# Kernel tuning notes

Hardware: AMD Instinct MI355X
Metric: run time of the kernel (lower is better)

## Reference

```python
import jax, jax.numpy as jnp
import numpy as np

L, B, F, D = 12, 2048, 6144, 768

def setup_inputs() -> dict:
    key = jax.random.key(0)
    k1, k2, k3 = jax.random.split(key, 3)
    acts = jax.random.normal(k1, (L, B, F), dtype=jnp.float32)
    # decoder weights for target layer: stacked per source layer, [L, F, D]
    W = jax.random.normal(k2, (L, F, D), dtype=jnp.float32) * 0.02
    bias = jax.random.normal(k3, (L, D), dtype=jnp.float32) * 0.01
    return {"acts": acts, "W": W, "bias": bias, "layer_idx": 11}

def reference(acts, W, bias, layer_idx):
    # decode(): sum over src_layer <= layer_idx of Linear(a[src], W[src->tgt], b[src->tgt])
    n = layer_idx + 1  # static Python int -> static slice
    a = acts[:n]       # [n, B, F]
    w = W[:n]          # [n, F, D]
    b = bias[:n]       # [n, D]
    # fused accumulation of all per-source-layer GEMMs
    recon = jnp.einsum('lbf,lfd->bd', a, w) + jnp.sum(b, axis=0)  # [B, D]
    return recon
```

## Files before the change

### kernel.cpp

```cpp
#include <hip/hip_runtime.h>
#include <hip/hip_bf16.h>

#define NB 2048
#define NF 6144
#define ND 768

typedef __attribute__((ext_vector_type(4))) __bf16 bf16x4;
typedef __attribute__((ext_vector_type(8))) __bf16 bf16x8;
typedef __attribute__((ext_vector_type(4))) float f32x4;

__global__ __launch_bounds__(256) void bias_init_kernel(
    const float* __restrict__ bias, const int* __restrict__ lidx,
    float* __restrict__ out) {
  int n = lidx[0] + 1;
  int i = blockIdx.x * 256 + threadIdx.x;
  if (i >= NB * ND) return;
  int d = i % ND;
  float s = 0.f;
  for (int l = 0; l < n; ++l) s += bias[l * ND + d];
  out[i] = s;
}

__global__ __launch_bounds__(256) void gemm_kernel(
    const float* __restrict__ acts, const float* __restrict__ W,
    const int* __restrict__ lidx, float* __restrict__ out) {
  const int l = blockIdx.z;
  if (l > lidx[0]) return;

  const int brow = blockIdx.x * 128;
  const int ncol = blockIdx.y * 128;

  __shared__ char cA[128 * 128];
  __shared__ char cB[128 * 128];

  const int tid = threadIdx.x;
  const int lane = tid & 63;
  const int wid = tid >> 6;
  const int wrow = (wid >> 1) * 64;
  const int wcol = (wid & 1) * 64;

  f32x4 acc[4][4];
#pragma unroll
  for (int i = 0; i < 4; ++i)
#pragma unroll
    for (int j = 0; j < 4; ++j) acc[i][j] = (f32x4){0.f, 0.f, 0.f, 0.f};

  const int arow = tid >> 4;
  const int ak = (tid & 15) * 4;
  const int bd = tid & 127;
  const int bkb0 = tid >> 7;

  const float* Aptr = acts + (size_t)l * NB * NF + (size_t)(brow + arow) * NF + ak;
  const float* Bptr = W + (size_t)l * NF * ND + (size_t)(bkb0 * 8) * ND + (ncol + bd);

  const int blkA = (ak >> 3) ^ (arow & 7);
  char* wA = cA + arow * 128 + (blkA << 4) + ((ak & 7) << 1);

  for (int kt = 0; kt < NF / 64; ++kt) {
    float4 av[8];
#pragma unroll
    for (int p = 0; p < 8; ++p)
      av[p] = *(const float4*)(Aptr + (size_t)p * (16 * NF));

    float bv[4][8];
#pragma unroll
    for (int p = 0; p < 4; ++p)
#pragma unroll
      for (int j = 0; j < 8; ++j)
        bv[p][j] = Bptr[(size_t)(p * 16 + j) * ND];

    __syncthreads();

#pragma unroll
    for (int p = 0; p < 8; ++p) {
      bf16x4 h;
      h[0] = (__bf16)av[p].x; h[1] = (__bf16)av[p].y;
      h[2] = (__bf16)av[p].z; h[3] = (__bf16)av[p].w;
      *(bf16x4*)(wA + p * 2048) = h;
    }
#pragma unroll
    for (int p = 0; p < 4; ++p) {
      const int kb8 = bkb0 + 2 * p;
      bf16x8 h;
#pragma unroll
      for (int j = 0; j < 8; ++j) h[j] = (__bf16)bv[p][j];
      *(bf16x8*)(cB + bd * 128 + ((kb8 ^ (bd & 7)) << 4)) = h;
    }

    __syncthreads();

#pragma unroll
    for (int s = 0; s < 2; ++s) {
      const int kb = s * 4 + (lane >> 4);
      bf16x8 aF[4], bF[4];
#pragma unroll
      for (int mi = 0; mi < 4; ++mi) {
        const int row = wrow + mi * 16 + (lane & 15);
        aF[mi] = *(const bf16x8*)(cA + row * 128 + ((kb ^ (row & 7)) << 4));
      }
#pragma unroll
      for (int ni = 0; ni < 4; ++ni) {
        const int row = wcol + ni * 16 + (lane & 15);
        bF[ni] = *(const bf16x8*)(cB + row * 128 + ((kb ^ (row & 7)) << 4));
      }
#pragma unroll
      for (int mi = 0; mi < 4; ++mi)
#pragma unroll
        for (int ni = 0; ni < 4; ++ni)
          acc[mi][ni] = __builtin_amdgcn_mfma_f32_16x16x32_bf16(
              aF[mi], bF[ni], acc[mi][ni], 0, 0, 0);
    }

    Aptr += 64;
    Bptr += (size_t)64 * ND;
  }

  const int orow = brow + wrow + ((lane >> 4) << 2);
  const int ocol = ncol + wcol + (lane & 15);
#pragma unroll
  for (int mi = 0; mi < 4; ++mi)
#pragma unroll
    for (int ni = 0; ni < 4; ++ni)
#pragma unroll
      for (int j = 0; j < 4; ++j)
        atomicAdd(out + (size_t)(orow + mi * 16 + j) * ND + (ocol + ni * 16),
                  acc[mi][ni][j]);
}

extern "C" void kernel_launch(void* const* d_in, const int* in_sizes, int n_in,
                              void* d_out, int out_size, void* d_ws, size_t ws_size,
                              hipStream_t stream) {
  const float* acts = (const float*)d_in[0];
  const float* W    = (const float*)d_in[1];
  const float* bias = (const float*)d_in[2];
  const int*   lidx = (const int*)d_in[3];
  float* out = (float*)d_out;

  const int L = in_sizes[0] / (NB * NF);

  bias_init_kernel<<<dim3((NB * ND + 255) / 256), 256, 0, stream>>>(bias, lidx, out);
  gemm_kernel<<<dim3(NB / 128, ND / 128, L), 256, 0, stream>>>(acts, W, lidx, out);
}
```

Measured before the change: 562.4 us.

## Software-pipeline global loads, vectorize W loads, and rework LDS swizzle

Global loads for the next K tile are issued right after the current tile is written to LDS, so they overlap with the MFMA compute instead of sitting in front of it. W is now read as float4 along the D dimension and transposed in registers, replacing scalar strided loads. A-tile stores widen to bf16x8. The LDS swizzle gains an extra XOR term, and launch bounds request two blocks per SIMD. The cost is that prefetch registers stay live across the compute loop, which adds register pressure.

Result: no change. 562.4 us (+0.0%).

```diff
diff --git a/kernel.cpp b/kernel.cpp
--- a/kernel.cpp
+++ b/kernel.cpp
@@ -4,10 +4,15 @@
 #define NB 2048
 #define NF 6144
 #define ND 768
+#define NT (NF / 64)
 
-typedef __attribute__((ext_vector_type(4))) __bf16 bf16x4;
 typedef __attribute__((ext_vector_type(8))) __bf16 bf16x8;
 typedef __attribute__((ext_vector_type(4))) float f32x4;
+
+__device__ __forceinline__ char* lds_addr(char* base, int row, int k) {
+  const int blk = ((k >> 3) ^ (row & 7) ^ ((row >> 2) & 7)) & 7;
+  return base + row * 128 + (blk << 4) + ((k & 7) << 1);
+}
 
 __global__ __launch_bounds__(256) void bias_init_kernel(
     const float* __restrict__ bias, const int* __restrict__ lidx,
@@ -21,7 +26,7 @@
   out[i] = s;
 }
 
-__global__ __launch_bounds__(256) void gemm_kernel(
+__global__ __launch_bounds__(256, 2) void gemm_kernel(
     const float* __restrict__ acts, const float* __restrict__ W,
     const int* __restrict__ lidx, float* __restrict__ out) {
   const int l = blockIdx.z;
@@ -45,64 +50,67 @@
 #pragma unroll
     for (int j = 0; j < 4; ++j) acc[i][j] = (f32x4){0.f, 0.f, 0.f, 0.f};
 
-  const int arow = tid >> 4;
-  const int ak = (tid & 15) * 4;
-  const int bd = tid & 127;
-  const int bkb0 = tid >> 7;
+  const int s_arow = tid >> 3;
+  const int s_ak = (tid & 7) * 8;
+  const int s_bd = (tid & 31) * 4;
+  const int s_bk = (tid >> 5) * 8;
 
-  const float* Aptr = acts + (size_t)l * NB * NF + (size_t)(brow + arow) * NF + ak;
-  const float* Bptr = W + (size_t)l * NF * ND + (size_t)(bkb0 * 8) * ND + (ncol + bd);
+  const float* Aptr =
+      acts + (size_t)l * NB * NF + (size_t)(brow + s_arow) * NF + s_ak;
+  const float* Bptr =
+      W + (size_t)l * NF * ND + (size_t)s_bk * ND + (ncol + s_bd);
 
-  const int blkA = (ak >> 3) ^ (arow & 7);
-  char* wA = cA + arow * 128 + (blkA << 4) + ((ak & 7) << 1);
+  float4 av[4][2];
+  float4 bv[8];
 
-  for (int kt = 0; kt < NF / 64; ++kt) {
-    float4 av[8];
+  auto LOADS = [&](int kb) {
 #pragma unroll
-    for (int p = 0; p < 8; ++p)
-      av[p] = *(const float4*)(Aptr + (size_t)p * (16 * NF));
-
-    float bv[4][8];
-#pragma unroll
-    for (int p = 0; p < 4; ++p)
-#pragma unroll
-      for (int j = 0; j < 8; ++j)
-        bv[p][j] = Bptr[(size_t)(p * 16 + j) * ND];
-
-    __syncthreads();
-
-#pragma unroll
-    for (int p = 0; p < 8; ++p) {
-      bf16x4 h;
-      h[0] = (__bf16)av[p].x; h[1] = (__bf16)av[p].y;
-      h[2] = (__bf16)av[p].z; h[3] = (__bf16)av[p].w;
-      *(bf16x4*)(wA + p * 2048) = h;
+    for (int p = 0; p < 4; ++p) {
+      av[p][0] = *(const float4*)(Aptr + (size_t)(32 * p) * NF + kb);
+      av[p][1] = *(const float4*)(Aptr + (size_t)(32 * p) * NF + kb + 4);
     }
 #pragma unroll
+    for (int j = 0; j < 8; ++j)
+      bv[j] = *(const float4*)(Bptr + (size_t)(kb + j) * ND);
+  };
+
+  auto STORE = [&]() {
+#pragma unroll
     for (int p = 0; p < 4; ++p) {
-      const int kb8 = bkb0 + 2 * p;
+      bf16x8 h;
+      h[0] = (__bf16)av[p][0].x; h[1] = (__bf16)av[p][0].y;
+      h[2] = (__bf16)av[p][0].z; h[3] = (__bf16)av[p][0].w;
+      h[4] = (__bf16)av[p][1].x; h[5] = (__bf16)av[p][1].y;
+      h[6] = (__bf16)av[p][1].z; h[7] = (__bf16)av[p][1].w;
+      *(bf16x8*)lds_addr(cA, s_arow + 32 * p, s_ak) = h;
+    }
+#pragma unroll
+    for (int dd = 0; dd < 4; ++dd) {
       bf16x8 h;
 #pragma unroll
-      for (int j = 0; j < 8; ++j) h[j] = (__bf16)bv[p][j];
-      *(bf16x8*)(cB + bd * 128 + ((kb8 ^ (bd & 7)) << 4)) = h;
+      for (int j = 0; j < 8; ++j) h[j] = (__bf16)bv[j][dd];
+      *(bf16x8*)lds_addr(cB, s_bd + dd, s_bk) = h;
     }
+  };
 
+  LOADS(0);
+
+  for (int kt = 0; kt < NT; ++kt) {
+    __syncthreads();
+    STORE();
+    if (kt + 1 < NT) LOADS((kt + 1) * 64);
     __syncthreads();
 
 #pragma unroll
     for (int s = 0; s < 2; ++s) {
-      const int kb = s * 4 + (lane >> 4);
+      const int kk = s * 32 + (lane >> 4) * 8;
       bf16x8 aF[4], bF[4];
 #pragma unroll
-      for (int mi = 0; mi < 4; ++mi) {
-        const int row = wrow + mi * 16 + (lane & 15);
-        aF[mi] = *(const bf16x8*)(cA + row * 128 + ((kb ^ (row & 7)) << 4));
-      }
+      for (int mi = 0; mi < 4; ++mi)
+        aF[mi] = *(const bf16x8*)lds_addr(cA, wrow + mi * 16 + (lane & 15), kk);
 #pragma unroll
-      for (int ni = 0; ni < 4; ++ni) {
-        const int row = wcol + ni * 16 + (lane & 15);
-        bF[ni] = *(const bf16x8*)(cB + row * 128 + ((kb ^ (row & 7)) << 4));
-      }
+      for (int ni = 0; ni < 4; ++ni)
+        bF[ni] = *(const bf16x8*)lds_addr(cB, wcol + ni * 16 + (lane & 15), kk);
 #pragma unroll
       for (int mi = 0; mi < 4; ++mi)
 #pragma unroll
@@ -110,9 +118,6 @@
           acc[mi][ni] = __builtin_amdgcn_mfma_f32_16x16x32_bf16(
               aF[mi], bF[ni], acc[mi][ni], 0, 0, 0);
     }
-
-    Aptr += 64;
-    Bptr += (size_t)64 * ND;
   }
 
   const int orow = brow + wrow + ((lane >> 4) << 2);
```
